# Optimization experiments

Measured on AMD Instinct MI355X. Metric: run time of the kernel, lower is better.

Reference implementation:

```python
import jax, jax.numpy as jnp
import numpy as np
from jax import lax

B, HI, WI, D = 8, 64, 64, 128
HO, WO = HI // 2, WI // 2
N_IN, N_OUT = HI * WI, HO * WO
NUM_ITERS = 3
EPS = 1e-6


def _build_indices(Ho, Wo):
    # replicates _build_q_and_in_idx: per coarse position, 9 relative offsets
    dys = np.repeat(np.arange(-1, 2), 3)
    dxs = np.tile(np.arange(-1, 2), 3)
    oy = np.arange(Ho)[:, None, None]
    ox = np.arange(Wo)[None, :, None]
    ny = oy + dys
    nx = ox + dxs
    valid = (ny >= 0) & (ny < Ho) & (nx >= 0) & (nx < Wo)  # (Ho,Wo,9)
    coarse = np.where(valid, ny * Wo + nx, 0)
    base = (oy * Wo + ox) * 9
    g9 = np.where(valid, base + np.arange(9), 0).reshape(-1, 9)
    c9 = coarse.reshape(-1, 9)
    q_idx = np.stack([np.tile(g9, (1, 4))] * 4)
    col_idx = np.stack([np.tile(c9, (1, 4))] * 4)
    in_idx = np.stack([np.tile(np.where(valid, coarse * 4 + h, 0).reshape(-1, 9), (1, 4)) for h in range(4)])
    return q_idx.astype(np.int32), in_idx.astype(np.int32), col_idx.astype(np.int32)


Q_IDX, IN_IDX, COL_IDX = _build_indices(HO, WO)
# NATTEN kernel-3 neighborhoods: window center clamped to stay in-bounds.
NY = np.clip(np.arange(HO) - 1, 0, HO - 3)[:, None] + np.arange(3)  # (HO,3)
NX = np.clip(np.arange(WO) - 1, 0, WO - 3)[:, None] + np.arange(3)  # (WO,3)


def _ln(x, g, b, eps=1e-5):
    mu = x.mean(-1, keepdims=True)
    var = ((x - mu) ** 2).mean(-1, keepdims=True)
    return (x - mu) * lax.rsqrt(var + eps) * g + b


def _forward(x, seed_w, wq, wk, wv, w1, b1, w2, b2, ln_in_g, ln_in_b, ln_out_g, ln_out_b, rpb, tau):
    ny, nx = jnp.asarray(NY), jnp.asarray(NX)
    q_idx = jnp.asarray(Q_IDX)

    def unfold(t):  # (B,HI,WI,D) -> (B,4,HO,WO,D); head = ky*2+kx (F.unfold order)
        return t.reshape(B, HO, 2, WO, 2, D).transpose(0, 2, 4, 1, 3, 5).reshape(B, 4, HO, WO, D)

    k = unfold((_ln(x, ln_in_g, ln_in_b) @ wk.T).reshape(B, HI, WI, D))
    v = unfold((x @ wv.T).reshape(B, HI, WI, D))
    k_n = k[:, :, ny][:, :, :, :, nx]  # (B,4,HO,3,WO,3,D)
    v_n = v[:, :, ny][:, :, :, :, nx]

    x_map = x.reshape(B, HI, WI, D).transpose(0, 3, 1, 2)
    seed = lax.conv_general_dilated(x_map, seed_w, (2, 2), ((1, 1), (1, 1)),
                                    dimension_numbers=('NCHW', 'OIHW', 'NCHW'))
    x_out = _ln(seed.reshape(B, D, N_OUT).transpose(0, 2, 1), ln_out_g, ln_out_b)

    scale = jnp.exp(tau)
    attn36 = a_col_h = None
    for _ in range(NUM_ITERS):
        q = (_ln(x_out, ln_out_g, ln_out_b) @ wq.T).reshape(B, HO, WO, D)
        # na2d_qk (q broadcast over the 4 heads) + relative position bias
        logits = jnp.einsum('byxd,bhykxld->bhyxkl', q, k_n).reshape(B, 4, HO, WO, 9) + rpb.reshape(1, 4, 1, 1, 9)
        attn = jax.nn.softmax(logits * scale, axis=-1) + EPS
        flat = attn.reshape(B, 4, N_OUT * 9)
        attn36 = jnp.take_along_axis(
            flat, jnp.broadcast_to(q_idx.reshape(1, 4, -1), (B, 4, N_OUT * 36)), axis=-1
        ).reshape(B, 4, N_OUT, 36)
        a_col_h = attn36 / (attn36.sum(axis=(1, 3), keepdims=True) + EPS)
        attn9 = a_col_h[..., :9].reshape(B, 4, HO, WO, 3, 3)
        # na2d_av then sum over heads
        updates = jnp.einsum('bhyxkl,bhykxld->byxd', attn9, v_n).reshape(B, N_OUT, D)
        x_out = x_out + updates
        h1 = jax.nn.gelu(x_out @ w1.T + b1, approximate=False)
        x_out = x_out + _ln(h1 @ w2.T + b2, ln_out_g, ln_out_b)
    return x_out, attn36, a_col_h


def setup_inputs() -> dict:
    key = jax.random.key(0)
    ks = jax.random.split(key, 8)
    n = lambda k, shape, s: jax.random.normal(k, shape, jnp.float32) * s
    D2 = 2 * D
    return {
        'x': jax.random.normal(ks[0], (B, N_IN, D), jnp.float32),
        'seed_w': n(ks[1], (D, D, 3, 3), (2.0 / (9 * D)) ** 0.5),
        'wq': n(ks[2], (D, D), D ** -0.5),
        'wk': n(ks[3], (D, D), D ** -0.5),
        'wv': n(ks[4], (D, D), D ** -0.5),
        'w1': n(ks[5], (D2, D), D ** -0.5),
        'b1': jnp.zeros((D2,), jnp.float32),
        'w2': n(ks[6], (D, D2), D2 ** -0.5),
        'b2': jnp.zeros((D,), jnp.float32),
        'ln_in_g': jnp.ones((D,), jnp.float32),
        'ln_in_b': jnp.zeros((D,), jnp.float32),
        'ln_out_g': jnp.ones((D,), jnp.float32),
        'ln_out_b': jnp.zeros((D,), jnp.float32),
        'rpb': n(ks[7], (4, 9), 0.02),
        'tau': jnp.float32(np.log(D ** -0.5)),
    }


def reference(x, seed_w, wq, wk, wv, w1, b1, w2, b2, ln_in_g, ln_in_b, ln_out_g, ln_out_b, rpb, tau):
    x_out, attn36, a_col_h = _forward(x, seed_w, wq, wk, wv, w1, b1, w2, b2,
                                      ln_in_g, ln_in_b, ln_out_g, ln_out_b, rpb, tau)
    # A_col: scatter_add over dim 1 -> A_col[b, in_idx[i,j], j] += a_col_h[b,i,j]
    rows = jnp.asarray(IN_IDX).reshape(4 * N_OUT, 36)
    cols = jnp.broadcast_to(jnp.arange(36), rows.shape)
    A_col = jnp.zeros((B, N_IN, N_OUT), x.dtype).at[:, rows, cols].add(a_col_h.reshape(B, 4 * N_OUT, 36))
    # A_row: scatter_add over dim 2 -> A_row[b, i, col_idx[i,j]] += attn36[b,i,j]
    ri = jnp.broadcast_to(jnp.arange(4 * N_OUT)[:, None], (4 * N_OUT, 36))
    A_row = jnp.zeros((B, N_IN, N_OUT), x.dtype).at[:, ri, jnp.asarray(COL_IDX).reshape(4 * N_OUT, 36)].add(
        attn36.reshape(B, 4 * N_OUT, 36))
    return x_out, A_row, A_col
```

## Files before the change

### kernel.cpp

```cpp
#include <hip/hip_runtime.h>
#include <hip/hip_bf16.h>
#include <math.h>

#define BB   8
#define HI_  64
#define WI_  64
#define DD   128
#define HO_  32
#define WO_  32
#define NIN  4096
#define NOUT 1024
#define LN_EPS 1e-5f
#define ATT_EPS 1e-6f

typedef short bf16x8 __attribute__((ext_vector_type(8)));
typedef float f32x4  __attribute__((ext_vector_type(4)));

__device__ __forceinline__ ushort f2bf(float f) {
    union { float f; unsigned u; } a; a.f = f;
    unsigned u = a.u;
    return (ushort)((u + 0x7FFFu + ((u >> 16) & 1u)) >> 16);
}
__device__ __forceinline__ float bf2f(ushort u) {
    union { unsigned u; float f; } a; a.u = ((unsigned)u) << 16;
    return a.f;
}

__global__ __launch_bounds__(256)
void wconvert_kernel(const float* __restrict__ wq, const float* __restrict__ wk,
                     const float* __restrict__ wv, const float* __restrict__ w1,
                     const float* __restrict__ w2, const float* __restrict__ sw,
                     ushort* __restrict__ dst)
{
    int i = blockIdx.x * 256 + threadIdx.x;
    float v;
    if (i < 16384)        v = wk[i];
    else if (i < 32768)   v = wv[i - 16384];
    else if (i < 49152) { int j = i - 32768; int d = j >> 7, n = j & 127;
                          v = wq[n * DD + d]; }
    else if (i < 81920)   v = w1[i - 49152];
    else if (i < 114688)  v = w2[i - 81920];
    else {
        int j = i - 114688;
        int n = j / 1152;
        int rem = j - n * 1152;
        int tap = rem >> 7, di = rem & 127;
        v = sw[((size_t)(n * DD + di)) * 9 + tap];
    }
    dst[i] = f2bf(v);
}

__global__ __launch_bounds__(256)
void prep_kernel(const float* __restrict__ x, const ushort* __restrict__ wkb,
                 const ushort* __restrict__ wvb, const ushort* __restrict__ wqTb,
                 const ushort* __restrict__ wcb,
                 const float* __restrict__ ligg, const float* __restrict__ libb,
                 const float* __restrict__ logg, const float* __restrict__ lobb,
                 ushort* __restrict__ k2buf, ushort* __restrict__ vbuf,
                 float* __restrict__ xout)
{
    __shared__ __align__(16) char arena[62208];
    const int tid = threadIdx.x;
    const int wid = tid >> 6, lane = tid & 63;
    const int lr = lane & 15, lk = (lane >> 4) << 3;

    if (blockIdx.x < 512) {
        ushort (*Araw)[136] = (ushort (*)[136])(arena);
        ushort (*Aln)[136]  = (ushort (*)[136])(arena + 17408);
        float  (*rstat)[2]  = (float  (*)[2])(arena + 34816);
        const int row0 = blockIdx.x * 64;

        float4 xv[8];
        #pragma unroll
        for (int i = 0; i < 8; ++i) {
            int l = tid + i * 256;
            int r = l >> 5, c4 = (l & 31) << 2;
            float4 v = *(const float4*)(x + (size_t)(row0 + r) * DD + c4);
            xv[i] = v;
            ushort4 o; o.x = f2bf(v.x); o.y = f2bf(v.y); o.z = f2bf(v.z); o.w = f2bf(v.w);
            *(ushort4*)&Araw[r][c4] = o;
            float s  = v.x + v.y + v.z + v.w;
            float s2 = v.x * v.x + v.y * v.y + v.z * v.z + v.w * v.w;
            #pragma unroll
            for (int o2 = 16; o2 > 0; o2 >>= 1) {
                s  += __shfl_down(s,  o2, 32);
                s2 += __shfl_down(s2, o2, 32);
            }
            if ((tid & 31) == 0) {
                float mu = s * (1.f / DD);
                float var = s2 * (1.f / DD) - mu * mu;
                rstat[r][0] = mu; rstat[r][1] = rsqrtf(var + LN_EPS);
            }
        }
        __syncthreads();
        #pragma unroll
        for (int i = 0; i < 8; ++i) {
            int l = tid + i * 256;
            int r = l >> 5, c4 = (l & 31) << 2;
            float mu = rstat[r][0], rs = rstat[r][1];
            float4 v = xv[i];
            ushort4 o;
            o.x = f2bf((v.x - mu) * rs * ligg[c4 + 0] + libb[c4 + 0]);
            o.y = f2bf((v.y - mu) * rs * ligg[c4 + 1] + libb[c4 + 1]);
            o.z = f2bf((v.z - mu) * rs * ligg[c4 + 2] + libb[c4 + 2]);
            o.w = f2bf((v.w - mu) * rs * ligg[c4 + 3] + libb[c4 + 3]);
            *(ushort4*)&Aln[r][c4] = o;
        }
        __syncthreads();

        const int wm = (wid & 1) * 32, wn = (wid >> 1) * 64;
        {
            f32x4 ak[2][4] = {}, av[2][4] = {};
            #pragma unroll
            for (int ks = 0; ks < 4; ++ks) {
                int kk = ks * 32 + lk;
                bf16x8 aL[2], aR[2];
                #pragma unroll
                for (int mi = 0; mi < 2; ++mi) {
                    aL[mi] = *(const bf16x8*)&Aln[wm + mi * 16 + lr][kk];
                    aR[mi] = *(const bf16x8*)&Araw[wm + mi * 16 + lr][kk];
                }
                #pragma unroll
                for (int ni = 0; ni < 4; ++ni) {
                    bf16x8 bK = *(const bf16x8*)(wkb + (size_t)(wn + ni * 16 + lr) * DD + kk);
                    bf16x8 bV = *(const bf16x8*)(wvb + (size_t)(wn + ni * 16 + lr) * DD + kk);
                    #pragma unroll
                    for (int mi = 0; mi < 2; ++mi) {
                        ak[mi][ni] = __builtin_amdgcn_mfma_f32_16x16x32_bf16(aL[mi], bK, ak[mi][ni], 0, 0, 0);
                        av[mi][ni] = __builtin_amdgcn_mfma_f32_16x16x32_bf16(aR[mi], bV, av[mi][ni], 0, 0, 0);
                    }
                }
            }
            #pragma unroll
            for (int mi = 0; mi < 2; ++mi)
                #pragma unroll
                for (int ni = 0; ni < 4; ++ni) {
                    int n = wn + ni * 16 + (lane & 15);
                    #pragma unroll
                    for (int r = 0; r < 4; ++r) {
                        int m = row0 + wm + mi * 16 + ((lane >> 4) << 2) + r;
                        int b = m >> 12, pix = m & 4095;
                        int iy = pix >> 6, ix = pix & 63;
                        int h = ((iy & 1) << 1) | (ix & 1);
                        int cp = ((iy >> 1) << 5) | (ix >> 1);
                        size_t orow = ((size_t)(b * 4 + h) << 10) + cp;
                        vbuf[orow * DD + n] = f2bf(av[mi][ni][r]);
                    }
                }
            __syncthreads();
            #pragma unroll
            for (int mi = 0; mi < 2; ++mi)
                #pragma unroll
                for (int ni = 0; ni < 4; ++ni) {
                    int n = wn + ni * 16 + (lane & 15);
                    #pragma unroll
                    for (int r = 0; r < 4; ++r) {
                        int lm = wm + mi * 16 + ((lane >> 4) << 2) + r;
                        Aln[lm][n] = f2bf(ak[mi][ni][r]);
                    }
                }
        }
        __syncthreads();

        {
            f32x4 a2[2][4] = {};
            #pragma unroll
            for (int ks = 0; ks < 4; ++ks) {
                int kk = ks * 32 + lk;
                bf16x8 aF[2];
                aF[0] = *(const bf16x8*)&Aln[wm + lr][kk];
                aF[1] = *(const bf16x8*)&Aln[wm + 16 + lr][kk];
                #pragma unroll
                for (int ni = 0; ni < 4; ++ni) {
                    bf16x8 bF = *(const bf16x8*)(wqTb + (size_t)(wn + ni * 16 + lr) * DD + kk);
                    a2[0][ni] = __builtin_amdgcn_mfma_f32_16x16x32_bf16(aF[0], bF, a2[0][ni], 0, 0, 0);
                    a2[1][ni] = __builtin_amdgcn_mfma_f32_16x16x32_bf16(aF[1], bF, a2[1][ni], 0, 0, 0);
                }
            }
            #pragma unroll
            for (int mi = 0; mi < 2; ++mi)
                #pragma unroll
                for (int ni = 0; ni < 4; ++ni) {
                    int n = wn + ni * 16 + (lane & 15);
                    #pragma unroll
                    for (int r = 0; r < 4; ++r) {
                        int m = row0 + wm + mi * 16 + ((lane >> 4) << 2) + r;
                        int b = m >> 12, pix = m & 4095;
                        int iy = pix >> 6, ix = pix & 63;
                        int h = ((iy & 1) << 1) | (ix & 1);
                        int cp = ((iy >> 1) << 5) | (ix >> 1);
                        size_t orow = ((size_t)(b * 4 + h) << 10) + cp;
                        k2buf[orow * DD + n] = f2bf(a2[mi][ni][r]);
                    }
                }
        }
    } else {
        ushort (*As)[72]   = (ushort (*)[72])(arena);
        ushort (*Bs)[72]   = (ushort (*)[72])(arena + 9216);
        float  (*es)[132]  = (float  (*)[132])(arena + 27648);
        float  (*rstat)[2] = (float  (*)[2])(arena + 61440);
        const int row0 = (blockIdx.x - 512) * 64;
        const int wm = (wid & 1) * 32, wn = (wid >> 1) * 64;
        f32x4 acc[2][4] = {};

        for (int k0 = 0; k0 < 1152; k0 += 64) {
            #pragma unroll
            for (int i = 0; i < 4; ++i) {
                int l = tid + i * 256;
                int r = l >> 4, c4 = (l & 15) << 2;
                int m = row0 + r;
                int b = m >> 10, p = m & 1023;
                int y = p >> 5, xx = p & 31;
                int kg = k0 + c4;
                int tap = kg >> 7, di = kg & 127;
                int ky = tap / 3, kx = tap - ky * 3;
                int iy = 2 * y + ky - 1, ix = 2 * xx + kx - 1;
                float4 v;
                if ((unsigned)iy < (unsigned)HI_ && (unsigned)ix < (unsigned)WI_)
                    v = *(const float4*)(x + ((size_t)b * NIN + iy * WI_ + ix) * DD + di);
                else v = make_float4(0.f, 0.f, 0.f, 0.f);
                ushort4 o; o.x = f2bf(v.x); o.y = f2bf(v.y); o.z = f2bf(v.z); o.w = f2bf(v.w);
                *(ushort4*)&As[r][c4] = o;
            }
            #pragma unroll
            for (int i = 0; i < 4; ++i) {
                int l = tid + i * 256;
                int r = l >> 3, c8 = (l & 7) << 3;
                *(uint4*)&Bs[r][c8] = *(const uint4*)(wcb + (size_t)r * 1152 + k0 + c8);
            }
            __syncthreads();
            #pragma unroll
            for (int ks = 0; ks < 2; ++ks) {
                int kk = ks * 32 + lk;
                bf16x8 aF[2];
                aF[0] = *(const bf16x8*)&As[wm + lr][kk];
                aF[1] = *(const bf16x8*)&As[wm + 16 + lr][kk];
                #pragma unroll
                for (int ni = 0; ni < 4; ++ni) {
                    bf16x8 bF = *(const bf16x8*)&Bs[wn + ni * 16 + lr][kk];
                    acc[0][ni] = __builtin_amdgcn_mfma_f32_16x16x32_bf16(aF[0], bF, acc[0][ni], 0, 0, 0);
                    acc[1][ni] = __builtin_amdgcn_mfma_f32_16x16x32_bf16(aF[1], bF, acc[1][ni], 0, 0, 0);
                }
            }
            __syncthreads();
        }
        #pragma unroll
        for (int mi = 0; mi < 2; ++mi)
            #pragma unroll
            for (int ni = 0; ni < 4; ++ni) {
                int n = wn + ni * 16 + (lane & 15);
                #pragma unroll
                for (int r = 0; r < 4; ++r)
                    es[wm + mi * 16 + ((lane >> 4) << 2) + r][n] = acc[mi][ni][r];
            }
        __syncthreads();
        {
            int r = tid >> 2, q = tid & 3;
            float s = 0.f, s2 = 0.f;
            #pragma unroll
            for (int c = 0; c < 32; ++c) { float v = es[r][q * 32 + c]; s += v; s2 += v * v; }
            s += __shfl_down(s, 1, 64); s2 += __shfl_down(s2, 1, 64);
            s += __shfl_down(s, 2, 64); s2 += __shfl_down(s2, 2, 64);
            if (q == 0) {
                float mu = s * (1.f / DD);
                float var = s2 * (1.f / DD) - mu * mu;
                rstat[r][0] = mu; rstat[r][1] = rsqrtf(var + LN_EPS);
            }
        }
        __syncthreads();
        #pragma unroll
        for (int i = 0; i < 8; ++i) {
            int l = tid + i * 256;
            int r = l >> 5, c4 = (l & 31) << 2;
            float mu = rstat[r][0], rs = rstat[r][1];
            float4 o;
            o.x = (es[r][c4 + 0] - mu) * rs * logg[c4 + 0] + lobb[c4 + 0];
            o.y = (es[r][c4 + 1] - mu) * rs * logg[c4 + 1] + lobb[c4 + 1];
            o.z = (es[r][c4 + 2] - mu) * rs * logg[c4 + 2] + lobb[c4 + 2];
            o.w = (es[r][c4 + 3] - mu) * rs * logg[c4 + 3] + lobb[c4 + 3];
            *(float4*)(xout + (size_t)(row0 + r) * DD + c4) = o;
        }
    }
}

template<int LAST>
__global__ __launch_bounds__(256)
void iter_kernel(float* __restrict__ xout, const ushort* __restrict__ k2buf,
                 const ushort* __restrict__ vbuf,
                 const ushort* __restrict__ w1b, const ushort* __restrict__ w2b,
                 const float* __restrict__ b1, const float* __restrict__ b2,
                 const float* __restrict__ lg_, const float* __restrict__ lb_,
                 const float* __restrict__ rpb, const float* __restrict__ tau,
                 float* __restrict__ gbuf, float* __restrict__ denb,
                 float* __restrict__ out)
{
    const int bid = blockIdx.x;
    const int b = bid >> 6, cy = (bid >> 1) & 31, cx0 = (bid & 1) << 4;
    const int ry0 = min(max(cy - 1, 0), HO_ - 3);
    const int tid = threadIdx.x;
    const int wid = tid >> 6, lane = tid & 63;
    const int lr = lane & 15, lk = (lane >> 4) << 3;

    __shared__ float  xsf[17][132];
    __shared__ ushort qs[17][136];
    __shared__ float  rstat[17][2];
    __shared__ float  lgp[16][36];
    __shared__ float  lg0[36];
    __shared__ float  sm0[4];
    __shared__ ushort h1s[16][264];
    __shared__ float  es[16][132];

    for (int l = tid; l < 544; l += 256) {
        int r = l >> 5, c4 = (l & 31) << 2;
        int g = b * NOUT + (r < 16 ? cy * 32 + cx0 + r : 0);
        *(float4*)&xsf[r][c4] = *(const float4*)(xout + (size_t)g * DD + c4);
    }
    __syncthreads();
    if (tid < 68) {
        int r = tid >> 2, q = tid & 3;
        float s = 0.f, s2 = 0.f;
        #pragma unroll
        for (int c = 0; c < 32; ++c) { float v = xsf[r][q * 32 + c]; s += v; s2 += v * v; }
        s += __shfl_down(s, 1, 64); s2 += __shfl_down(s2, 1, 64);
        s += __shfl_down(s, 2, 64); s2 += __shfl_down(s2, 2, 64);
        if (q == 0) {
            float mu = s * (1.f / DD);
            float var = s2 * (1.f / DD) - mu * mu;
            rstat[r][0] = mu; rstat[r][1] = rsqrtf(var + LN_EPS);
        }
    }
    __syncthreads();
    for (int l = tid; l < 544; l += 256) {
        int r = l >> 5, c4 = (l & 31) << 2;
        float mu = rstat[r][0], rs = rstat[r][1];
        ushort4 o;
        o.x = f2bf((xsf[r][c4 + 0] - mu) * rs * lg_[c4 + 0] + lb_[c4 + 0]);
        o.y = f2bf((xsf[r][c4 + 1] - mu) * rs * lg_[c4 + 1] + lb_[c4 + 1]);
        o.z = f2bf((xsf[r][c4 + 2] - mu) * rs * lg_[c4 + 2] + lb_[c4 + 2]);
        o.w = f2bf((xsf[r][c4 + 3] - mu) * rs * lg_[c4 + 3] + lb_[c4 + 3]);
        *(ushort4*)&qs[r][c4] = o;
    }
    __syncthreads();

    for (int task = tid; task < 612; task += 256) {
        const ushort *kp, *qp;
        int cl = 0, h, jj;
        if (task < 576) {
            cl = task / 36; int t2 = task - cl * 36;
            h = t2 / 9; jj = t2 - h * 9;
            int ky = jj / 3, kx = jj - ky * 3;
            int c = cx0 + cl;
            int nx = min(max(c - 1, 0), WO_ - 3) + kx;
            kp = k2buf + (((size_t)(b * 4 + h) << 10) + (ry0 + ky) * 32 + nx) * DD;
            qp = &qs[cl][0];
        } else {
            int t2 = task - 576;
            h = t2 / 9; jj = t2 - h * 9;
            int ky = jj / 3, kx = jj - ky * 3;
            kp = k2buf + (((size_t)(b * 4 + h) << 10) + ky * 32 + kx) * DD;
            qp = &qs[16][0];
        }
        float s = 0.f;
        #pragma unroll 4
        for (int d = 0; d < 128; d += 8) {
            uint4 ku = *(const uint4*)(kp + d);
            uint4 qu = *(const uint4*)(qp + d);
            const ushort* kk2 = (const ushort*)&ku;
            const ushort* qq2 = (const ushort*)&qu;
            #pragma unroll
            for (int t = 0; t < 8; ++t) s += bf2f(kk2[t]) * bf2f(qq2[t]);
        }
        if (task < 576) lgp[cl][h * 9 + jj] = s;
        else            lg0[task - 576] = s;
    }
    __syncthreads();

    if (tid < 68) {
        float scale = expf(tau[0]);
        int h; const float* lptr; int cl = 0;
        if (tid < 64) { cl = tid >> 2; h = tid & 3; lptr = &lgp[cl][h * 9]; }
        else          { h = tid - 64; lptr = &lg0[h * 9]; }
        float tmpv[9], mx = -1e30f;
        #pragma unroll
        for (int jj = 0; jj < 9; ++jj) {
            float v = (lptr[jj] + rpb[h * 9 + jj]) * scale;
            tmpv[jj] = v; mx = fmaxf(mx, v);
        }
        float ss = 0.f;
        #pragma unroll
        for (int jj = 0; jj < 9; ++jj) { tmpv[jj] = expf(tmpv[jj] - mx); ss += tmpv[jj]; }
        float inv = 1.f / ss;
        if (tid < 64) {
            #pragma unroll
            for (int jj = 0; jj < 9; ++jj) lgp[cl][h * 9 + jj] = tmpv[jj] * inv + ATT_EPS;
        } else sm0[h] = tmpv[0] * inv + ATT_EPS;
    }
    __syncthreads();

    if (tid < 64) {
        int cl = tid >> 2, h = tid & 3;
        int c = cx0 + cl;
        float s = 0.f, gv[9];
        #pragma unroll
        for (int jj = 0; jj < 9; ++jj) {
            int dy = jj / 3 - 1, dx = jj % 3 - 1;
            bool valid = ((unsigned)(cy + dy) < (unsigned)HO_) && ((unsigned)(c + dx) < (unsigned)WO_);
            float v = valid ? lgp[cl][h * 9 + jj] : sm0[h];
            gv[jj] = v; s += v;
        }
        float tot = s;
        tot += __shfl_xor(tot, 1, 4);
        tot += __shfl_xor(tot, 2, 4);
        float dd = 4.f * tot + ATT_EPS;
        if (h == 0) denb[b * NOUT + cy * 32 + cx0 + cl] = dd;
        float inv = 1.f / dd;
        float* gp = gbuf + (((size_t)(b * 4 + h) << 10) + cy * 32 + c) * 9;
        #pragma unroll
        for (int jj = 0; jj < 9; ++jj) {
            gp[jj] = gv[jj];
            lgp[cl][h * 9 + jj] = gv[jj] * inv;
        }
    }
    __syncthreads();

    {
        int cl = tid >> 4, d0 = (tid & 15) << 3;
        int c = cx0 + cl;
        int rx0 = min(max(c - 1, 0), WO_ - 3);
        float acc8[8] = {};
        #pragma unroll
        for (int h = 0; h < 4; ++h)
            #pragma unroll
            for (int jj = 0; jj < 9; ++jj) {
                float cf = lgp[cl][h * 9 + jj];
                int ky = jj / 3, kx = jj - ky * 3;
                const ushort* vp = vbuf + (((size_t)(b * 4 + h) << 10) + (ry0 + ky) * 32 + rx0 + kx) * DD + d0;
                uint4 v0 = *(const uint4*)(vp);
                const ushort* vs0 = (const ushort*)&v0;
                #pragma unroll
                for (int t = 0; t < 8; ++t) acc8[t] += cf * bf2f(vs0[t]);
            }
        #pragma unroll
        for (int t = 0; t < 8; t += 4) {
            float4 o = *(float4*)&xsf[cl][d0 + t];
            o.x += acc8[t]; o.y += acc8[t + 1]; o.z += acc8[t + 2]; o.w += acc8[t + 3];
            *(float4*)&xsf[cl][d0 + t] = o;
        }
    }
    __syncthreads();

    for (int l = tid; l < 512; l += 256) {
        int r = l >> 5, c4 = (l & 31) << 2;
        ushort4 o;
        o.x = f2bf(xsf[r][c4 + 0]); o.y = f2bf(xsf[r][c4 + 1]);
        o.z = f2bf(xsf[r][c4 + 2]); o.w = f2bf(xsf[r][c4 + 3]);
        *(ushort4*)&qs[r][c4] = o;
    }
    __syncthreads();
    {
        const int wn = wid * 64;
        f32x4 acc[4] = {};
        #pragma unroll
        for (int ks = 0; ks < 4; ++ks) {
            int kk = ks * 32 + lk;
            bf16x8 a0 = *(const bf16x8*)&qs[lr][kk];
            #pragma unroll
            for (int ni = 0; ni < 4; ++ni) {
                bf16x8 bF = *(const bf16x8*)(w1b + (size_t)(wn + ni * 16 + lr) * DD + kk);
                acc[ni] = __builtin_amdgcn_mfma_f32_16x16x32_bf16(a0, bF, acc[ni], 0, 0, 0);
            }
        }
        #pragma unroll
        for (int ni = 0; ni < 4; ++ni) {
            int n = wn + ni * 16 + (lane & 15);
            float bv = b1[n];
            #pragma unroll
            for (int r = 0; r < 4; ++r) {
                int m = ((lane >> 4) << 2) + r;
                float v = acc[ni][r] + bv;
                v = 0.5f * v * (1.f + erff(v * 0.70710678118654752f));
                h1s[m][n] = f2bf(v);
            }
        }
    }
    __syncthreads();

    {
        const int wn = wid * 32;
        f32x4 acc[2] = {};
        #pragma unroll
        for (int ks = 0; ks < 8; ++ks) {
            int kk = ks * 32 + lk;
            bf16x8 a0 = *(const bf16x8*)&h1s[lr][kk];
            #pragma unroll
            for (int ni = 0; ni < 2; ++ni) {
                bf16x8 bF = *(const bf16x8*)(w2b + (size_t)(wn + ni * 16 + lr) * 256 + kk);
                acc[ni] = __builtin_amdgcn_mfma_f32_16x16x32_bf16(a0, bF, acc[ni], 0, 0, 0);
            }
        }
        #pragma unroll
        for (int ni = 0; ni < 2; ++ni) {
            int n = wn + ni * 16 + (lane & 15);
            float bv = b2[n];
            #pragma unroll
            for (int r = 0; r < 4; ++r)
                es[((lane >> 4) << 2) + r][n] = acc[ni][r] + bv;
        }
    }
    __syncthreads();
    if (tid < 128) {
        int r = tid >> 3, qq = tid & 7;
        float s = 0.f, s2 = 0.f;
        #pragma unroll
        for (int c = 0; c < 16; ++c) { float v = es[r][qq * 16 + c]; s += v; s2 += v * v; }
        s += __shfl_down(s, 1, 64); s2 += __shfl_down(s2, 1, 64);
        s += __shfl_down(s, 2, 64); s2 += __shfl_down(s2, 2, 64);
        s += __shfl_down(s, 4, 64); s2 += __shfl_down(s2, 4, 64);
        if (qq == 0) {
            float mu = s * (1.f / DD);
            float var = s2 * (1.f / DD) - mu * mu;
            rstat[r][0] = mu; rstat[r][1] = rsqrtf(var + LN_EPS);
        }
    }
    __syncthreads();
    for (int l = tid; l < 512; l += 256) {
        int r = l >> 5, c4 = (l & 31) << 2;
        float mu = rstat[r][0], rs = rstat[r][1];
        size_t off = ((size_t)(b * NOUT + cy * 32 + cx0 + r)) * DD + c4;
        float4 o;
        o.x = xsf[r][c4 + 0] + (es[r][c4 + 0] - mu) * rs * lg_[c4 + 0] + lb_[c4 + 0];
        o.y = xsf[r][c4 + 1] + (es[r][c4 + 1] - mu) * rs * lg_[c4 + 1] + lb_[c4 + 1];
        o.z = xsf[r][c4 + 2] + (es[r][c4 + 2] - mu) * rs * lg_[c4 + 2] + lb_[c4 + 2];
        o.w = xsf[r][c4 + 3] + (es[r][c4 + 3] - mu) * rs * lg_[c4 + 3] + lb_[c4 + 3];
        *(float4*)(xout + off) = o;
        if (LAST) *(float4*)(out + off) = o;
    }
}

__global__ __launch_bounds__(256)
void arowcol_kernel(const float* __restrict__ gbuf, const float* __restrict__ denb,
                    float* __restrict__ Arow, float* __restrict__ Acol)
{
    const int tid = threadIdx.x;
    __shared__ int   cols[9];
    __shared__ float vals[9];
    __shared__ float wred[9][4];
    if (blockIdx.x < 32768) {
        const int bi = blockIdx.x;
        const int b = bi >> 12, i = bi & 4095;
        const int h = i >> 10, p = i & 1023;
        const int cy = p >> 5, cx = p & 31;
        if (tid < 9) {
            int dy = tid / 3 - 1, dx = tid % 3 - 1;
            bool valid = ((unsigned)(cy + dy) < (unsigned)HO_) && ((unsigned)(cx + dx) < (unsigned)WO_);
            cols[tid] = valid ? (cy + dy) * WO_ + (cx + dx) : 0;
            vals[tid] = 4.f * gbuf[(((size_t)(b * 4 + h) << 10) + p) * 9 + tid];
        }
        __syncthreads();
        float* row = Arow + (size_t)bi * NOUT;
        int c4 = tid << 2;
        float o[4] = {};
        #pragma unroll
        for (int e = 0; e < 4; ++e)
            #pragma unroll
            for (int jj = 0; jj < 9; ++jj)
                if (cols[jj] == c4 + e) o[e] += vals[jj];
        *(float4*)(row + c4) = make_float4(o[0], o[1], o[2], o[3]);
    } else {
        const int br = blockIdx.x - 32768;
        const int b = br >> 12, r = br & 4095;
        const int h = r & 3, coarse = r >> 2;
        const int cy = coarse >> 5, cx = coarse & 31;
        if (tid < 9) {
            int dy = tid / 3 - 1, dx = tid % 3 - 1;
            int py = cy - dy, px = cx - dx;
            float v = 0.f;
            if ((unsigned)py < (unsigned)HO_ && (unsigned)px < (unsigned)WO_) {
                int p = py * WO_ + px;
                v = gbuf[(((size_t)(b * 4 + h) << 10) + p) * 9 + tid] / denb[b * NOUT + p];
            }
            vals[tid] = v;
        }
        if (r == 0) {
            float part[9] = {};
            for (int p = tid; p < NOUT; p += 256) {
                float invd = 1.f / denb[b * NOUT + p];
                int py = p >> 5, px = p & 31;
                #pragma unroll
                for (int jj = 0; jj < 9; ++jj) {
                    int dy = jj / 3 - 1, dx = jj % 3 - 1;
                    bool valid = ((unsigned)(py + dy) < (unsigned)HO_) && ((unsigned)(px + dx) < (unsigned)WO_);
                    if (!valid) part[jj] += invd;
                }
            }
            #pragma unroll
            for (int jj = 0; jj < 9; ++jj) {
                float s = part[jj];
                #pragma unroll
                for (int o = 32; o > 0; o >>= 1) s += __shfl_down(s, o, 64);
                if ((tid & 63) == 0) wred[jj][tid >> 6] = s;
            }
            __syncthreads();
            if (tid < 9) {
                float s = wred[tid][0] + wred[tid][1] + wred[tid][2] + wred[tid][3];
                float H = 0.f;
                for (int h2 = 0; h2 < 4; ++h2)
                    H += gbuf[(((size_t)(b * 4 + h2)) << 10) * 9];
                vals[tid] += H * s;
            }
        }
        __syncthreads();
        float* row = Acol + (size_t)br * NOUT;
        int c4 = tid << 2;
        float o[4];
        #pragma unroll
        for (int e = 0; e < 4; ++e) {
            int c = c4 + e;
            o[e] = (c < 36) ? vals[c % 9] : 0.f;
        }
        *(float4*)(row + c4) = make_float4(o[0], o[1], o[2], o[3]);
    }
}

extern "C" void kernel_launch(void* const* d_in, const int* in_sizes, int n_in,
                              void* d_out, int out_size, void* d_ws, size_t ws_size,
                              hipStream_t stream)
{
    const float* x        = (const float*)d_in[0];
    const float* seed_w   = (const float*)d_in[1];
    const float* wq       = (const float*)d_in[2];
    const float* wk       = (const float*)d_in[3];
    const float* wv       = (const float*)d_in[4];
    const float* w1       = (const float*)d_in[5];
    const float* b1       = (const float*)d_in[6];
    const float* w2       = (const float*)d_in[7];
    const float* b2       = (const float*)d_in[8];
    const float* ln_in_g  = (const float*)d_in[9];
    const float* ln_in_b  = (const float*)d_in[10];
    const float* ln_out_g = (const float*)d_in[11];
    const float* ln_out_b = (const float*)d_in[12];
    const float* rpb      = (const float*)d_in[13];
    const float* tau      = (const float*)d_in[14];

    float* out  = (float*)d_out;
    float* Arow = out + (size_t)BB * NOUT * DD;
    float* Acol = Arow + (size_t)BB * NIN * NOUT;

    float* ws    = (float*)d_ws;
    float* xout  = ws;
    float* gbuf  = xout + (size_t)BB * NOUT * DD;
    float* denb  = gbuf + (size_t)BB * 4 * NOUT * 9;
    ushort* wb   = (ushort*)(denb + BB * NOUT);
    ushort* wkb  = wb;
    ushort* wvb  = wb + 16384;
    ushort* wqTb = wb + 32768;
    ushort* w1b  = wb + 49152;
    ushort* w2b  = wb + 81920;
    ushort* wcb  = wb + 114688;

    ushort* k2buf = (ushort*)Arow;
    ushort* vbuf  = k2buf + (size_t)4194304;

    wconvert_kernel<<<1024, 256, 0, stream>>>(wq, wk, wv, w1, w2, seed_w, wb);
    prep_kernel<<<640, 256, 0, stream>>>(x, wkb, wvb, wqTb, wcb, ln_in_g, ln_in_b,
                                         ln_out_g, ln_out_b, k2buf, vbuf, xout);

    for (int it = 0; it < 3; ++it) {
        if (it < 2)
            iter_kernel<0><<<BB * HO_ * 2, 256, 0, stream>>>(
                xout, k2buf, vbuf, w1b, w2b, b1, b2, ln_out_g, ln_out_b,
                rpb, tau, gbuf, denb, out);
        else
            iter_kernel<1><<<BB * HO_ * 2, 256, 0, stream>>>(
                xout, k2buf, vbuf, w1b, w2b, b1, b2, ln_out_g, ln_out_b,
                rpb, tau, gbuf, denb, out);
    }

    arowcol_kernel<<<2 * BB * NIN, 256, 0, stream>>>(gbuf, denb, Arow, Acol);
}
```

Before: 191.9 us.

## Spread dense A_row/A_col zero-fill across earlier kernels and write sparse entries only

The dense zeroing of the large A_row and most of A_col is moved into the prep and iteration kernels, each of which clears a slice alongside its compute. The final kernel then writes only the nonzero entries, plus a few special rows, instead of streaming every row. The K/V staging buffers move into the tail of A_col, which those kernels leave uncleared and the finish kernel overwrites. The iteration kernel also fuses the two softmax passes into one and fuses the residual update with the bf16 conversion, removing barriers. The aim is to overlap the large output-write bandwidth with compute-bound phases. The risk is that the ordering of zero-fill and sparse writes must line up correctly across kernels.

```diff
diff --git a/kernel.cpp b/kernel.cpp
--- a/kernel.cpp
+++ b/kernel.cpp
@@ -12,6 +12,8 @@
 #define NOUT 1024
 #define LN_EPS 1e-5f
 #define ATT_EPS 1e-6f
+
+#define ZSHARE 3932160
 
 typedef short bf16x8 __attribute__((ext_vector_type(8)));
 typedef float f32x4  __attribute__((ext_vector_type(4)));
@@ -57,12 +59,19 @@
                  const float* __restrict__ ligg, const float* __restrict__ libb,
                  const float* __restrict__ logg, const float* __restrict__ lobb,
                  ushort* __restrict__ k2buf, ushort* __restrict__ vbuf,
-                 float* __restrict__ xout)
+                 float* __restrict__ xout, float4* __restrict__ zb)
 {
     __shared__ __align__(16) char arena[62208];
     const int tid = threadIdx.x;
     const int wid = tid >> 6, lane = tid & 63;
     const int lr = lane & 15, lk = (lane >> 4) << 3;
+
+    {
+        float4* zp = zb + (size_t)blockIdx.x * 6144;
+        float4 zz = make_float4(0.f, 0.f, 0.f, 0.f);
+        #pragma unroll
+        for (int i = 0; i < 24; ++i) zp[i * 256 + tid] = zz;
+    }
 
     if (blockIdx.x < 512) {
         ushort (*Araw)[136] = (ushort (*)[136])(arena);
@@ -292,7 +301,7 @@
                  const float* __restrict__ lg_, const float* __restrict__ lb_,
                  const float* __restrict__ rpb, const float* __restrict__ tau,
                  float* __restrict__ gbuf, float* __restrict__ denb,
-                 float* __restrict__ out)
+                 float* __restrict__ out, float4* __restrict__ zb)
 {
     const int bid = blockIdx.x;
     const int b = bid >> 6, cy = (bid >> 1) & 31, cx0 = (bid & 1) << 4;
@@ -306,9 +315,15 @@
     __shared__ float  rstat[17][2];
     __shared__ float  lgp[16][36];
     __shared__ float  lg0[36];
-    __shared__ float  sm0[4];
     __shared__ ushort h1s[16][264];
     __shared__ float  es[16][132];
+
+    {
+        float4* zp = zb + (size_t)blockIdx.x * 7680;
+        float4 zz = make_float4(0.f, 0.f, 0.f, 0.f);
+        #pragma unroll
+        for (int i = 0; i < 30; ++i) zp[i * 256 + tid] = zz;
+    }
 
     for (int l = tid; l < 544; l += 256) {
         int r = l >> 5, c4 = (l & 31) << 2;
@@ -375,37 +390,36 @@
     }
     __syncthreads();
 
-    if (tid < 68) {
-        float scale = expf(tau[0]);
-        int h; const float* lptr; int cl = 0;
-        if (tid < 64) { cl = tid >> 2; h = tid & 3; lptr = &lgp[cl][h * 9]; }
-        else          { h = tid - 64; lptr = &lg0[h * 9]; }
-        float tmpv[9], mx = -1e30f;
-        #pragma unroll
-        for (int jj = 0; jj < 9; ++jj) {
-            float v = (lptr[jj] + rpb[h * 9 + jj]) * scale;
-            tmpv[jj] = v; mx = fmaxf(mx, v);
-        }
-        float ss = 0.f;
-        #pragma unroll
-        for (int jj = 0; jj < 9; ++jj) { tmpv[jj] = expf(tmpv[jj] - mx); ss += tmpv[jj]; }
-        float inv = 1.f / ss;
-        if (tid < 64) {
-            #pragma unroll
-            for (int jj = 0; jj < 9; ++jj) lgp[cl][h * 9 + jj] = tmpv[jj] * inv + ATT_EPS;
-        } else sm0[h] = tmpv[0] * inv + ATT_EPS;
-    }
-    __syncthreads();
-
     if (tid < 64) {
         int cl = tid >> 2, h = tid & 3;
         int c = cx0 + cl;
+        float scale = expf(tau[0]);
+        float tmpv[9], mx = -1e30f;
+        #pragma unroll
+        for (int jj = 0; jj < 9; ++jj) {
+            float v = (lgp[cl][h * 9 + jj] + rpb[h * 9 + jj]) * scale;
+            tmpv[jj] = v; mx = fmaxf(mx, v);
+        }
+        float ss = 0.f;
+        #pragma unroll
+        for (int jj = 0; jj < 9; ++jj) { tmpv[jj] = expf(tmpv[jj] - mx); ss += tmpv[jj]; }
+        float inv = 1.f / ss;
+        float t0[9], mx0 = -1e30f;
+        #pragma unroll
+        for (int jj = 0; jj < 9; ++jj) {
+            float v = (lg0[h * 9 + jj] + rpb[h * 9 + jj]) * scale;
+            t0[jj] = v; mx0 = fmaxf(mx0, v);
+        }
+        float ss0 = 0.f;
+        #pragma unroll
+        for (int jj = 0; jj < 9; ++jj) ss0 += expf(t0[jj] - mx0);
+        float sm0v = expf(t0[0] - mx0) / ss0 + ATT_EPS;
         float s = 0.f, gv[9];
         #pragma unroll
         for (int jj = 0; jj < 9; ++jj) {
             int dy = jj / 3 - 1, dx = jj % 3 - 1;
             bool valid = ((unsigned)(cy + dy) < (unsigned)HO_) && ((unsigned)(c + dx) < (unsigned)WO_);
-            float v = valid ? lgp[cl][h * 9 + jj] : sm0[h];
+            float v = valid ? (tmpv[jj] * inv + ATT_EPS) : sm0v;
             gv[jj] = v; s += v;
         }
         float tot = s;
@@ -413,12 +427,12 @@
         tot += __shfl_xor(tot, 2, 4);
         float dd = 4.f * tot + ATT_EPS;
         if (h == 0) denb[b * NOUT + cy * 32 + cx0 + cl] = dd;
-        float inv = 1.f / dd;
+        float invd = 1.f / dd;
         float* gp = gbuf + (((size_t)(b * 4 + h) << 10) + cy * 32 + c) * 9;
         #pragma unroll
         for (int jj = 0; jj < 9; ++jj) {
             gp[jj] = gv[jj];
-            lgp[cl][h * 9 + jj] = gv[jj] * inv;
+            lgp[cl][h * 9 + jj] = gv[jj] * invd;
         }
     }
     __syncthreads();
@@ -440,23 +454,20 @@
                 #pragma unroll
                 for (int t = 0; t < 8; ++t) acc8[t] += cf * bf2f(vs0[t]);
             }
-        #pragma unroll
-        for (int t = 0; t < 8; t += 4) {
-            float4 o = *(float4*)&xsf[cl][d0 + t];
-            o.x += acc8[t]; o.y += acc8[t + 1]; o.z += acc8[t + 2]; o.w += acc8[t + 3];
-            *(float4*)&xsf[cl][d0 + t] = o;
-        }
-    }
-    __syncthreads();
-
-    for (int l = tid; l < 512; l += 256) {
-        int r = l >> 5, c4 = (l & 31) << 2;
-        ushort4 o;
-        o.x = f2bf(xsf[r][c4 + 0]); o.y = f2bf(xsf[r][c4 + 1]);
-        o.z = f2bf(xsf[r][c4 + 2]); o.w = f2bf(xsf[r][c4 + 3]);
-        *(ushort4*)&qs[r][c4] = o;
-    }
-    __syncthreads();
+        float nv[8];
+        #pragma unroll
+        for (int t = 0; t < 8; ++t) nv[t] = xsf[cl][d0 + t] + acc8[t];
+        #pragma unroll
+        for (int t = 0; t < 8; t += 4)
+            *(float4*)&xsf[cl][d0 + t] = make_float4(nv[t], nv[t+1], nv[t+2], nv[t+3]);
+        ushort4 q0, q1;
+        q0.x = f2bf(nv[0]); q0.y = f2bf(nv[1]); q0.z = f2bf(nv[2]); q0.w = f2bf(nv[3]);
+        q1.x = f2bf(nv[4]); q1.y = f2bf(nv[5]); q1.z = f2bf(nv[6]); q1.w = f2bf(nv[7]);
+        *(ushort4*)&qs[cl][d0]     = q0;
+        *(ushort4*)&qs[cl][d0 + 4] = q1;
+    }
+    __syncthreads();
+
     {
         const int wn = wid * 64;
         f32x4 acc[4] = {};
@@ -532,45 +543,109 @@
         o.y = xsf[r][c4 + 1] + (es[r][c4 + 1] - mu) * rs * lg_[c4 + 1] + lb_[c4 + 1];
         o.z = xsf[r][c4 + 2] + (es[r][c4 + 2] - mu) * rs * lg_[c4 + 2] + lb_[c4 + 2];
         o.w = xsf[r][c4 + 3] + (es[r][c4 + 3] - mu) * rs * lg_[c4 + 3] + lb_[c4 + 3];
-        *(float4*)(xout + off) = o;
         if (LAST) *(float4*)(out + off) = o;
+        else      *(float4*)(xout + off) = o;
     }
 }
 
 __global__ __launch_bounds__(256)
-void arowcol_kernel(const float* __restrict__ gbuf, const float* __restrict__ denb,
-                    float* __restrict__ Arow, float* __restrict__ Acol)
+void sparse_finish_kernel(const float* __restrict__ gbuf, const float* __restrict__ denb,
+                          float* __restrict__ Arow, float* __restrict__ Acol)
 {
     const int tid = threadIdx.x;
-    __shared__ int   cols[9];
-    __shared__ float vals[9];
-    __shared__ float wred[9][4];
-    if (blockIdx.x < 32768) {
-        const int bi = blockIdx.x;
-        const int b = bi >> 12, i = bi & 4095;
-        const int h = i >> 10, p = i & 1023;
-        const int cy = p >> 5, cx = p & 31;
+    if (blockIdx.x < 128) {
+        int row = blockIdx.x * 256 + tid;
+        int b = row >> 12, i = row & 4095;
+        int h = i >> 10, p = i & 1023;
+        int cy = p >> 5, cx = p & 31;
+        const float* gp = gbuf + (((size_t)(b * 4 + h) << 10) + p) * 9;
+        float* rowp = Arow + (size_t)row * NOUT;
+        float acc0 = 0.f; bool has0 = false;
+        #pragma unroll
+        for (int jj = 0; jj < 9; ++jj) {
+            int dy = jj / 3 - 1, dx = jj % 3 - 1;
+            bool valid = ((unsigned)(cy + dy) < (unsigned)HO_) && ((unsigned)(cx + dx) < (unsigned)WO_);
+            float g4 = 4.f * gp[jj];
+            int col = (cy + dy) * WO_ + (cx + dx);
+            if (valid && col != 0) rowp[col] = g4;
+            else { acc0 += g4; has0 = true; }
+        }
+        if (has0) rowp[0] = acc0;
+    } else if (blockIdx.x < 240) {
+        int br = (blockIdx.x - 128) * 256 + tid;
+        int b = br >> 12, r = br & 4095;
+        if (r != 0) {
+            int h = r & 3, coarse = r >> 2;
+            int cy = coarse >> 5, cx = coarse & 31;
+            float val[9];
+            #pragma unroll
+            for (int jj = 0; jj < 9; ++jj) {
+                int dy = jj / 3 - 1, dx = jj % 3 - 1;
+                int py = cy - dy, px = cx - dx;
+                float v = 0.f;
+                if ((unsigned)py < (unsigned)HO_ && (unsigned)px < (unsigned)WO_) {
+                    int p = py * WO_ + px;
+                    v = gbuf[(((size_t)(b * 4 + h) << 10) + p) * 9 + jj] / denb[b * NOUT + p];
+                }
+                val[jj] = v;
+            }
+            float* rowp = Acol + (size_t)br * NOUT;
+            #pragma unroll
+            for (int q = 0; q < 9; ++q) {
+                float4 o = make_float4(val[(4 * q) % 9], val[(4 * q + 1) % 9],
+                                       val[(4 * q + 2) % 9], val[(4 * q + 3) % 9]);
+                *(float4*)(rowp + 4 * q) = o;
+            }
+        }
+    } else if (blockIdx.x < 247) {
+        const int b = blockIdx.x - 240;
+        __shared__ float vals[9];
+        __shared__ float wred[9][4];
         if (tid < 9) {
             int dy = tid / 3 - 1, dx = tid % 3 - 1;
-            bool valid = ((unsigned)(cy + dy) < (unsigned)HO_) && ((unsigned)(cx + dx) < (unsigned)WO_);
-            cols[tid] = valid ? (cy + dy) * WO_ + (cx + dx) : 0;
-            vals[tid] = 4.f * gbuf[(((size_t)(b * 4 + h) << 10) + p) * 9 + tid];
+            int py = -dy, px = -dx;
+            float v = 0.f;
+            if ((unsigned)py < (unsigned)HO_ && (unsigned)px < (unsigned)WO_) {
+                int p = py * WO_ + px;
+                v = gbuf[(((size_t)(b * 4 + 0) << 10) + p) * 9 + tid] / denb[b * NOUT + p];
+            }
+            vals[tid] = v;
+        }
+        float part[9] = {};
+        for (int p = tid; p < NOUT; p += 256) {
+            float invd = 1.f / denb[b * NOUT + p];
+            int py = p >> 5, px = p & 31;
+            #pragma unroll
+            for (int jj = 0; jj < 9; ++jj) {
+                int dy = jj / 3 - 1, dx = jj % 3 - 1;
+                bool valid = ((unsigned)(py + dy) < (unsigned)HO_) && ((unsigned)(px + dx) < (unsigned)WO_);
+                if (!valid) part[jj] += invd;
+            }
+        }
+        #pragma unroll
+        for (int jj = 0; jj < 9; ++jj) {
+            float s = part[jj];
+            #pragma unroll
+            for (int o = 32; o > 0; o >>= 1) s += __shfl_down(s, o, 64);
+            if ((tid & 63) == 0) wred[jj][tid >> 6] = s;
         }
         __syncthreads();
-        float* row = Arow + (size_t)bi * NOUT;
-        int c4 = tid << 2;
-        float o[4] = {};
-        #pragma unroll
-        for (int e = 0; e < 4; ++e)
-            #pragma unroll
-            for (int jj = 0; jj < 9; ++jj)
-                if (cols[jj] == c4 + e) o[e] += vals[jj];
-        *(float4*)(row + c4) = make_float4(o[0], o[1], o[2], o[3]);
+        if (tid < 9) {
+            float s = wred[tid][0] + wred[tid][1] + wred[tid][2] + wred[tid][3];
+            float H = 0.f;
+            for (int h2 = 0; h2 < 4; ++h2)
+                H += gbuf[(((size_t)(b * 4 + h2)) << 10) * 9];
+            vals[tid] += H * s;
+        }
+        __syncthreads();
+        if (tid < 36) Acol[(size_t)(b * 4096) * NOUT + tid] = vals[tid % 9];
     } else {
-        const int br = blockIdx.x - 32768;
+        const int br = 28672 + (blockIdx.x - 247);
         const int b = br >> 12, r = br & 4095;
         const int h = r & 3, coarse = r >> 2;
         const int cy = coarse >> 5, cx = coarse & 31;
+        __shared__ float vals[9];
+        __shared__ float wred[9][4];
         if (tid < 9) {
             int dy = tid / 3 - 1, dx = tid % 3 - 1;
             int py = cy - dy, px = cx - dx;
@@ -610,7 +685,7 @@
             }
         }
         __syncthreads();
-        float* row = Acol + (size_t)br * NOUT;
+        float* rowp = Acol + (size_t)br * NOUT;
         int c4 = tid << 2;
         float o[4];
         #pragma unroll
@@ -618,7 +693,7 @@
             int c = c4 + e;
             o[e] = (c < 36) ? vals[c % 9] : 0.f;
         }
-        *(float4*)(row + c4) = make_float4(o[0], o[1], o[2], o[3]);
+        *(float4*)(rowp + c4) = make_float4(o[0], o[1], o[2], o[3]);
     }
 }
 
@@ -645,6 +720,7 @@
     float* out  = (float*)d_out;
     float* Arow = out + (size_t)BB * NOUT * DD;
     float* Acol = Arow + (size_t)BB * NIN * NOUT;
+    float4* zb  = (float4*)Arow;
 
     float* ws    = (float*)d_ws;
     float* xout  = ws;
@@ -658,23 +734,23 @@
     ushort* w2b  = wb + 81920;
     ushort* wcb  = wb + 114688;
 
-    ushort* k2buf = (ushort*)Arow;
+    ushort* k2buf = (ushort*)(Acol + (size_t)28672 * NOUT);
     ushort* vbuf  = k2buf + (size_t)4194304;
 
     wconvert_kernel<<<1024, 256, 0, stream>>>(wq, wk, wv, w1, w2, seed_w, wb);
     prep_kernel<<<640, 256, 0, stream>>>(x, wkb, wvb, wqTb, wcb, ln_in_g, ln_in_b,
-                                         ln_out_g, ln_out_b, k2buf, vbuf, xout);
-
-    for (int it = 0; it < 3; ++it) {
-        if (it < 2)
-            iter_kernel<0><<<BB * HO_ * 2, 256, 0, stream>>>(
-                xout, k2buf, vbuf, w1b, w2b, b1, b2, ln_out_g, ln_out_b,
-                rpb, tau, gbuf, denb, out);
-        else
-            iter_kernel<1><<<BB * HO_ * 2, 256, 0, stream>>>(
-                xout, k2buf, vbuf, w1b, w2b, b1, b2, ln_out_g, ln_out_b,
-                rpb, tau, gbuf, denb, out);
-    }
-
-    arowcol_kernel<<<2 * BB * NIN, 256, 0, stream>>>(gbuf, denb, Arow, Acol);
+                                         ln_out_g, ln_out_b, k2buf, vbuf, xout,
+                                         zb + (size_t)0 * ZSHARE);
+
+    iter_kernel<0><<<BB * HO_ * 2, 256, 0, stream>>>(
+        xout, k2buf, vbuf, w1b, w2b, b1, b2, ln_out_g, ln_out_b,
+        rpb, tau, gbuf, denb, out, zb + (size_t)1 * ZSHARE);
+    iter_kernel<0><<<BB * HO_ * 2, 256, 0, stream>>>(
+        xout, k2buf, vbuf, w1b, w2b, b1, b2, ln_out_g, ln_out_b,
+        rpb, tau, gbuf, denb, out, zb + (size_t)2 * ZSHARE);
+    iter_kernel<1><<<BB * HO_ * 2, 256, 0, stream>>>(
+        xout, k2buf, vbuf, w1b, w2b, b1, b2, ln_out_g, ln_out_b,
+        rpb, tau, gbuf, denb, out, zb + (size_t)3 * ZSHARE);
+
+    sparse_finish_kernel<<<4343, 256, 0, stream>>>(gbuf, denb, Arow, Acol);
 }
```

Result: faster. 179.5 us (-6.5%).
